# Kernel tuning notes

Measured on AMD Instinct MI355X. Metric: run time of the kernel, lower is better.

Reference implementation:

```python
import jax, jax.numpy as jnp
import numpy as np
from jax import lax

B, L, D, E, K, H = 8, 1024, 256, 8, 2, 1024  # batch, seq(in_channel), in_dim, experts, top_k, out_channel/hidden
LMAX = L // 2  # largest expert input dim (factor i+2 = 2)
LENS = [L // (i + 2) for i in range(E)]


def setup_inputs() -> dict:
    key = jax.random.key(0)
    ks = jax.random.split(key, 12)
    x = jax.random.normal(ks[0], (B, L, D), dtype=jnp.float32)
    conv_ws = jax.random.normal(ks[1], (3, D, D, 3), dtype=jnp.float32) / np.sqrt(3 * D)
    conv_bs = jax.random.normal(ks[2], (3, D), dtype=jnp.float32) * 0.01
    fl_w = jax.random.normal(ks[3], (E, L), dtype=jnp.float32) / np.sqrt(L)
    fl_b = jax.random.normal(ks[4], (E,), dtype=jnp.float32) * 0.01
    # expert first-layer weights, zero-padded on input axis to LMAX (expert i uses L//(i+2) inputs)
    w1 = jax.random.normal(ks[5], (E, H, LMAX), dtype=jnp.float32) / np.sqrt(LMAX)
    col_mask = (np.arange(LMAX)[None, :] < np.array(LENS)[:, None]).astype(np.float32)  # [E, LMAX]
    w1 = w1 * jnp.asarray(col_mask)[:, None, :]
    b1 = jax.random.normal(ks[6], (E, H), dtype=jnp.float32) * 0.01
    w2 = jax.random.normal(ks[7], (E, H, H), dtype=jnp.float32) / np.sqrt(H)
    b2 = jax.random.normal(ks[8], (E, H), dtype=jnp.float32) * 0.01
    w3 = jax.random.normal(ks[9], (E, H, H), dtype=jnp.float32) / np.sqrt(H)
    b3 = jax.random.normal(ks[10], (E, H), dtype=jnp.float32) * 0.01
    return {"x": x, "conv_ws": conv_ws, "conv_bs": conv_bs, "fl_w": fl_w, "fl_b": fl_b,
            "w1": w1, "b1": b1, "w2": w2, "b2": b2, "w3": w3, "b3": b3}


def _gelu(v):
    return jax.nn.gelu(v, approximate=False)  # torch nn.GELU default is exact erf


def _forward(x, conv_ws, conv_bs, fl_w, fl_b, w1, b1, w2, b2, w3, b3):
    xt = jnp.transpose(x, (0, 2, 1))  # [B, D, L]
    # --- Router: 3 dilated causal-padded ('same') convs + GELU ---
    h = xt
    for i in range(3):
        d = 2 ** i
        h = lax.conv_general_dilated(h, conv_ws[i], window_strides=(1,), padding=[(d, d)],
                                     rhs_dilation=(d,), dimension_numbers=("NCH", "OIH", "NCH"))
        h = _gelu(h + conv_bs[i][None, :, None])
    logits = jax.nn.sigmoid(jnp.einsum("bdl,el->bde", h, fl_w) + fl_b)  # [B, D, E]
    prob = jax.nn.softmax(logits, axis=-1)
    top_val, top_idx = lax.top_k(prob, K)  # [B, D, K]
    top_val = top_val / jnp.sum(top_val, axis=-1, keepdims=True)
    # combine gate per expert: gates[b,d,e] = sum_k top_val * 1[top_idx==e]
    gates = jnp.sum(top_val[..., None] * jax.nn.one_hot(top_idx, E, dtype=top_val.dtype), axis=2)  # [B, D, E]
    # --- Per-expert downsample (avg_pool1d, kernel=stride=i+2), zero-padded to LMAX ---
    xs = []
    for i in range(E):
        f = i + 2
        Li = LENS[i]
        xd = xt[:, :, :Li * f].reshape(B, D, Li, f).mean(-1)  # [B, D, Li]
        xs.append(jnp.pad(xd, ((0, 0), (0, 0), (0, LMAX - Li))))
    xe = jnp.stack(xs)  # [E, B, D, LMAX]; pad cols align with zeroed w1 cols
    # --- Expert MLPs (dense compute, masked by gates; zero gate == token not routed) ---
    h1 = _gelu(jnp.einsum("ebdl,ehl->ebdh", xe, w1) + b1[:, None, None, :])
    h2 = _gelu(jnp.einsum("ebdh,egh->ebdg", h1, w2) + b2[:, None, None, :])
    h3 = jnp.einsum("ebdg,eog->ebdo", h2, w3) + b3[:, None, None, :]  # [E, B, D, H]
    out = jnp.einsum("ebdo,bde->bdo", h3, gates)  # scatter-add combine, [B, D, H]
    return jnp.transpose(out, (0, 2, 1))  # [B, L(out_channel), D]


def reference(x, conv_ws, conv_bs, fl_w, fl_b, w1, b1, w2, b2, w3, b3):
    return _forward(x, conv_ws, conv_bs, fl_w, fl_b, w1, b1, w2, b2, w3, b3)
```

## Files before the change

kernel.cpp:

```cpp
#include <hip/hip_runtime.h>
#include <math.h>

#define Bb 8
#define Ll 1024
#define Dd 256
#define Ee 8
#define Hh 1024
#define LMAXc 512
#define NTOK (Bb*Dd)
#define LPAD 1032
#define MAXTILES 72

typedef short bf16x8 __attribute__((ext_vector_type(8)));
typedef float f32x4 __attribute__((ext_vector_type(4)));
typedef unsigned short u16x8 __attribute__((ext_vector_type(8)));

__device__ __forceinline__ float gelu_f(float x) {
    return 0.5f * x * (1.0f + erff(x * 0.70710678118654752440f));
}
__device__ __forceinline__ unsigned short f2b(float x) {
    unsigned int u = __float_as_uint(x);
    return (unsigned short)((u + 0x7fffu + ((u >> 16) & 1u)) >> 16);
}
__device__ __forceinline__ float b2f(unsigned short h) {
    return __uint_as_float(((unsigned int)h) << 16);
}
__device__ __forceinline__ void gl_lds16(const void* g, void* l) {
    __builtin_amdgcn_global_load_lds((const __attribute__((address_space(1))) unsigned int*)g,
                                     (__attribute__((address_space(3))) unsigned int*)l, 16, 0, 0);
}

__global__ __launch_bounds__(256) void prep_all(
    const float* __restrict__ x, const float* __restrict__ cw,
    unsigned short* __restrict__ xhi, unsigned short* __restrict__ xlo,
    unsigned short* __restrict__ chi, unsigned short* __restrict__ clo,
    unsigned short* __restrict__ wchi, unsigned short* __restrict__ wclo,
    unsigned short* __restrict__ xe)
{
    int blk = blockIdx.x;
    int t = threadIdx.x;
    if (blk < 4096) {
        int u = blk;
        int e = u >> 9;
        int b = (u >> 6) & 7;
        int c = u & 63;
        int f = e + 2;
        int Li = Ll / f;
        int j0 = c * 8;
        if (j0 >= Li) return;
        int d = t;
        float invf = 1.0f / (float)f;
        int lim = Li - 1;
        float v[8] = {};
        for (int r = 0; r < f; ++r) {
            #pragma unroll
            for (int jj = 0; jj < 8; ++jj) {
                int j = j0 + jj; if (j > lim) j = lim;
                v[jj] += x[((size_t)(b * Ll + j * f + r)) * Dd + d];
            }
        }
        size_t obase = ((size_t)(e * NTOK + b * 256 + d)) * LMAXc + j0;
        if (j0 + 8 <= Li) {
            u16x8 hv;
            #pragma unroll
            for (int q = 0; q < 8; ++q) hv[q] = (short)f2b(v[q] * invf);
            *(u16x8*)(xe + obase) = hv;
        } else {
            for (int jj = 0; jj < Li - j0; ++jj)
                xe[obase + jj] = f2b(v[jj] * invf);
        }
    } else if (blk < 4128) {
        int u = (blk - 4096) * 256 + t;
        int f = u >> 11;
        int rem = u & 2047;
        int b = rem >> 8;
        int r2 = rem & 255;
        int row = r2 >> 5;
        int col = (r2 & 31) * 8;
        int padrow = (row < 4) ? row : (1024 + row);
        unsigned short* buf = (f == 0) ? xhi : (f == 1) ? xlo : (f == 2) ? chi : clo;
        u16x8 z = {0, 0, 0, 0, 0, 0, 0, 0};
        *(u16x8*)(buf + (size_t)(b * LPAD + padrow) * Dd + col) = z;
    } else if (blk < 4384) {
        int cb = blk - 4128;
        const float4* s4 = (const float4*)x;
        size_t ob = (size_t)cb * 1024 + t;
        float4 v[8];
        #pragma unroll
        for (int it = 0; it < 4; ++it) {
            v[2 * it]     = s4[(ob + it * 256) * 2];
            v[2 * it + 1] = s4[(ob + it * 256) * 2 + 1];
        }
        #pragma unroll
        for (int it = 0; it < 4; ++it) {
            size_t o = ob + it * 256;
            int d8 = (int)(o & 31), l = (int)((o >> 5) & 1023), b = (int)(o >> 15);
            size_t ooff = (size_t)(b * LPAD + 4 + l) * Dd + d8 * 8;
            float vv[8] = {v[2*it].x, v[2*it].y, v[2*it].z, v[2*it].w,
                           v[2*it+1].x, v[2*it+1].y, v[2*it+1].z, v[2*it+1].w};
            u16x8 hv, lv;
            #pragma unroll
            for (int q = 0; q < 8; ++q) {
                unsigned short h = f2b(vv[q]);
                hv[q] = (short)h;
                lv[q] = (short)f2b(vv[q] - b2f(h));
            }
            *(u16x8*)(xhi + ooff) = hv;
            *(u16x8*)(xlo + ooff) = lv;
        }
    } else {
        int cb = blk - 4384;
        int idx0 = (cb * 256 + t) * 8;
        float vv[8];
        #pragma unroll
        for (int q = 0; q < 8; ++q) {
            int idx = idx0 + q;
            int i = idx & (Dd - 1);
            int o = (idx >> 8) & (Dd - 1);
            int lk = idx >> 16;
            int layer = lk / 3;
            int k = lk % 3;
            vv[q] = cw[(((size_t)layer * Dd + o) * Dd + i) * 3 + k];
        }
        u16x8 hv, lv;
        #pragma unroll
        for (int q = 0; q < 8; ++q) {
            unsigned short h = f2b(vv[q]);
            hv[q] = (short)h;
            lv[q] = (short)f2b(vv[q] - b2f(h));
        }
        *(u16x8*)(wchi + idx0) = hv;
        *(u16x8*)(wclo + idx0) = lv;
    }
}

template<int MODE, int CVT>
__global__ __launch_bounds__(256, 2) void conv_mfma(
    const unsigned short* __restrict__ inhi, const unsigned short* __restrict__ inlo,
    const unsigned short* __restrict__ whiL, const unsigned short* __restrict__ wloL,
    const float* __restrict__ bias,
    unsigned short* __restrict__ outhi, unsigned short* __restrict__ outlo,
    const float* __restrict__ flw, float* __restrict__ logits,
    const float* __restrict__ cvsrc, unsigned short* __restrict__ cvd1,
    unsigned short* __restrict__ cvd2, int dil)
{
    __shared__ char smem[32768];

    if (CVT && blockIdx.y >= (Dd / 64)) {
        int cb = (blockIdx.y - Dd / 64) * 128 + blockIdx.x;
        int t = threadIdx.x;
        const float4* s4 = (const float4*)cvsrc;
        size_t ob = (size_t)cb * 1024 + t;
        float4 v[8];
        #pragma unroll
        for (int it = 0; it < 4; ++it) {
            v[2 * it]     = s4[(ob + it * 256) * 2];
            v[2 * it + 1] = s4[(ob + it * 256) * 2 + 1];
        }
        #pragma unroll
        for (int it = 0; it < 4; ++it) {
            size_t o = ob + it * 256;
            float vv[8] = {v[2*it].x, v[2*it].y, v[2*it].z, v[2*it].w,
                           v[2*it+1].x, v[2*it+1].y, v[2*it+1].z, v[2*it+1].w};
            u16x8 hv, lv;
            #pragma unroll
            for (int q = 0; q < 8; ++q) {
                unsigned short h = f2b(vv[q]);
                hv[q] = (short)h;
                if (CVT == 1) lv[q] = (short)f2b(vv[q] - b2f(h));
            }
            *(u16x8*)(cvd1 + o * 8) = hv;
            if (CVT == 1) *(u16x8*)(cvd2 + o * 8) = lv;
        }
        return;
    }

    char* sAhi = smem;
    char* sAlo = smem + 8192;
    char* sBhi = smem + 16384;
    char* sBlo = smem + 24576;

    const int t = threadIdx.x;
    const int lane = t & 63, w = t >> 6;
    const int r16 = lane & 15, quad = lane >> 4;
    const int wr = w >> 1, wc = w & 1;
    const int row0 = blockIdx.x * 64;
    const int col0 = blockIdx.y * 64;
    const int b = row0 >> 10, l0 = row0 & 1023;

    int aoff[2], boff[2];
    #pragma unroll
    for (int i = 0; i < 2; ++i) {
        int ra = wr * 32 + i * 16 + r16;
        aoff[i] = ra * 64 + ((quad ^ ((ra >> 1) & 3)) << 4);
        int rb = wc * 32 + i * 16 + r16;
        boff[i] = rb * 64 + ((quad ^ ((rb >> 1) & 3)) << 4);
    }
    const int rs = t >> 2, ce = ((t & 3) ^ ((rs >> 1) & 3)) << 3;
    const unsigned short* gAhi = inhi + (size_t)(b * LPAD + 4 + l0 + rs) * Dd + ce;
    const unsigned short* gAlo = inlo + (size_t)(b * LPAD + 4 + l0 + rs) * Dd + ce;

    f32x4 acc[2][2];
    const f32x4 zero4 = {0.f, 0.f, 0.f, 0.f};
    #pragma unroll
    for (int i = 0; i < 2; ++i)
        #pragma unroll
        for (int j = 0; j < 2; ++j) acc[i][j] = zero4;

    for (int tap = 0; tap < 3; ++tap) {
        const int sh = (tap - 1) * dil;
        const unsigned short* pAhi = gAhi + sh * Dd;
        const unsigned short* pAlo = gAlo + sh * Dd;
        const unsigned short* gBhi = whiL + ((size_t)tap * Dd + col0 + rs) * Dd + ce;
        const unsigned short* gBlo = wloL + ((size_t)tap * Dd + col0 + rs) * Dd + ce;
        for (int kb = 0; kb < Dd; kb += 64) {
            gl_lds16(pAhi + kb,      sAhi + (w << 10));
            gl_lds16(pAhi + kb + 32, sAhi + 4096 + (w << 10));
            gl_lds16(pAlo + kb,      sAlo + (w << 10));
            gl_lds16(pAlo + kb + 32, sAlo + 4096 + (w << 10));
            gl_lds16(gBhi + kb,      sBhi + (w << 10));
            gl_lds16(gBhi + kb + 32, sBhi + 4096 + (w << 10));
            gl_lds16(gBlo + kb,      sBlo + (w << 10));
            gl_lds16(gBlo + kb + 32, sBlo + 4096 + (w << 10));
            __syncthreads();
            #pragma unroll
            for (int h = 0; h < 2; ++h) {
                const int ho = h * 4096;
                bf16x8 ah[2], al[2], bh[2], bl[2];
                #pragma unroll
                for (int i = 0; i < 2; ++i) {
                    ah[i] = *(const bf16x8*)(sAhi + ho + aoff[i]);
                    al[i] = *(const bf16x8*)(sAlo + ho + aoff[i]);
                    bh[i] = *(const bf16x8*)(sBhi + ho + boff[i]);
                    bl[i] = *(const bf16x8*)(sBlo + ho + boff[i]);
                }
                #pragma unroll
                for (int mi = 0; mi < 2; ++mi)
                    #pragma unroll
                    for (int ni = 0; ni < 2; ++ni) {
                        acc[mi][ni] = __builtin_amdgcn_mfma_f32_16x16x32_bf16(ah[mi], bh[ni], acc[mi][ni], 0, 0, 0);
                        acc[mi][ni] = __builtin_amdgcn_mfma_f32_16x16x32_bf16(ah[mi], bl[ni], acc[mi][ni], 0, 0, 0);
                        acc[mi][ni] = __builtin_amdgcn_mfma_f32_16x16x32_bf16(al[mi], bh[ni], acc[mi][ni], 0, 0, 0);
                    }
            }
            __syncthreads();
        }
    }

    int cc[2]; float bv[2];
    #pragma unroll
    for (int ni = 0; ni < 2; ++ni) {
        cc[ni] = col0 + wc * 32 + ni * 16 + r16;
        bv[ni] = bias[cc[ni]];
    }
    if (MODE == 0) {
        #pragma unroll
        for (int mi = 0; mi < 2; ++mi) {
            int lb = l0 + wr * 32 + mi * 16 + quad * 4;
            #pragma unroll
            for (int reg = 0; reg < 4; ++reg) {
                int l = lb + reg;
                #pragma unroll
                for (int ni = 0; ni < 2; ++ni) {
                    float v = gelu_f(acc[mi][ni][reg] + bv[ni]);
                    size_t o = (size_t)(b * LPAD + 4 + l) * Dd + cc[ni];
                    unsigned short h = f2b(v);
                    outhi[o] = h;
                    outlo[o] = f2b(v - b2f(h));
                }
            }
        }
    } else {
        float* wl   = (float*)smem;
        float* slog = (float*)(smem + 2048);
        for (int i = t; i < 512; i += 256) {
            int ll = i >> 3, e = i & 7;
            wl[i] = flw[e * Ll + l0 + ll];
            slog[i] = 0.0f;
        }
        __syncthreads();
        float part[2][8];
        #pragma unroll
        for (int ni = 0; ni < 2; ++ni)
            #pragma unroll
            for (int e = 0; e < 8; ++e) part[ni][e] = 0.0f;
        #pragma unroll
        for (int mi = 0; mi < 2; ++mi) {
            #pragma unroll
            for (int reg = 0; reg < 4; ++reg) {
                int ll = wr * 32 + mi * 16 + quad * 4 + reg;
                #pragma unroll
                for (int ni = 0; ni < 2; ++ni) {
                    float v = gelu_f(acc[mi][ni][reg] + bv[ni]);
                    #pragma unroll
                    for (int e = 0; e < 8; ++e) part[ni][e] += v * wl[ll * 8 + e];
                }
            }
        }
        #pragma unroll
        for (int ni = 0; ni < 2; ++ni) {
            int dl = wc * 32 + ni * 16 + r16;
            #pragma unroll
            for (int e = 0; e < 8; ++e) atomicAdd(&slog[dl * 8 + e], part[ni][e]);
        }
        __syncthreads();
        for (int i = t; i < 512; i += 256) {
            int dl = i >> 3, e = i & 7;
            atomicAdd(&logits[(size_t)(b * Dd + col0 + dl) * Ee + e], slog[i]);
        }
    }
}

template<int MODE, int GATHER, int TWOPASS>
__global__ __launch_bounds__(256, 4) void gemm_sp(
    const unsigned short* __restrict__ AG,
    const unsigned short* __restrict__ BhiG, const unsigned short* __restrict__ BloG,
    const float* __restrict__ biasG, const float* __restrict__ gates,
    const int* __restrict__ cntG, const int* __restrict__ listG,
    const int* __restrict__ tileTab, const int* __restrict__ ntiles,
    unsigned short* __restrict__ Cout, float* __restrict__ outf,
    int M, int N, int K)
{
    if (blockIdx.y >= ntiles[0]) return;
    const int desc = tileTab[blockIdx.y];
    const int e = desc >> 16;
    const int row0 = (desc & 0xffff) * 64;
    const int cn = cntG[e];

    constexpr int NCH = TWOPASS ? 2 : 4;
    __shared__ char smem[TWOPASS ? 24576 : 32768];
    char* sA   = smem;
    char* sBhi = smem + NCH * 4096;
    char* sBlo = smem + 2 * NCH * 4096;

    const unsigned short* Bhi = BhiG + (size_t)e * N * K;
    const unsigned short* Blo = TWOPASS ? (BloG + (size_t)e * N * K) : nullptr;
    const float* bias = biasG + (size_t)e * N;

    int Keff = K;
    if (GATHER) {
        int Li = Ll / (e + 2);
        Keff = ((Li + 63) >> 6) << 6;
    }

    const int t = threadIdx.x;
    const int lane = t & 63, w = t >> 6;
    const int r16 = lane & 15, quad = lane >> 4;
    const int wr = w >> 1, wc = w & 1;
    const int col0 = blockIdx.x * 64;

    int aoff[2], boff[2];
    #pragma unroll
    for (int i = 0; i < 2; ++i) {
        int ra = wr * 32 + i * 16 + r16;
        aoff[i] = ra * 64 + ((quad ^ ((ra >> 1) & 3)) << 4);
        int rb = wc * 32 + i * 16 + r16;
        boff[i] = rb * 64 + ((quad ^ ((rb >> 1) & 3)) << 4);
    }
    const int r0s = t >> 2, c0s = ((t & 3) ^ ((r0s >> 1) & 3)) << 3;
    int ri = row0 + r0s; if (ri > cn - 1) ri = cn - 1;
    const int ar = GATHER ? listG[e * NTOK + ri] : ri;
    const unsigned short* gA  = AG + ((size_t)e * M + ar) * K + c0s;
    const unsigned short* gB  = Bhi + (size_t)(col0 + r0s) * K + c0s;
    const unsigned short* gBl = TWOPASS ? (Blo + (size_t)(col0 + r0s) * K + c0s) : nullptr;
    const int wofs = w << 10;

    f32x4 acc[2][2];
    const f32x4 zero4 = {0.f, 0.f, 0.f, 0.f};
    #pragma unroll
    for (int i = 0; i < 2; ++i)
        #pragma unroll
        for (int j = 0; j < 2; ++j) acc[i][j] = zero4;

    for (int k0 = 0; k0 < Keff; k0 += NCH * 32) {
        #pragma unroll
        for (int c = 0; c < NCH; ++c) {
            gl_lds16(gA + k0 + c * 32, sA + c * 4096 + wofs);
            gl_lds16(gB + k0 + c * 32, sBhi + c * 4096 + wofs);
        }
        if (TWOPASS) {
            #pragma unroll
            for (int c = 0; c < NCH; ++c)
                gl_lds16(gBl + k0 + c * 32, sBlo + c * 4096 + wofs);
        }
        __syncthreads();
        #pragma unroll
        for (int h = 0; h < NCH; ++h) {
            const int ho = h * 4096;
            bf16x8 ah[2], bh[2];
            #pragma unroll
            for (int i = 0; i < 2; ++i) {
                ah[i] = *(const bf16x8*)(sA + ho + aoff[i]);
                bh[i] = *(const bf16x8*)(sBhi + ho + boff[i]);
            }
            #pragma unroll
            for (int mi = 0; mi < 2; ++mi)
                #pragma unroll
                for (int ni = 0; ni < 2; ++ni)
                    acc[mi][ni] = __builtin_amdgcn_mfma_f32_16x16x32_bf16(ah[mi], bh[ni], acc[mi][ni], 0, 0, 0);
            if (TWOPASS) {
                bf16x8 bl[2];
                #pragma unroll
                for (int i = 0; i < 2; ++i) bl[i] = *(const bf16x8*)(sBlo + ho + boff[i]);
                #pragma unroll
                for (int mi = 0; mi < 2; ++mi)
                    #pragma unroll
                    for (int ni = 0; ni < 2; ++ni)
                        acc[mi][ni] = __builtin_amdgcn_mfma_f32_16x16x32_bf16(ah[mi], bl[ni], acc[mi][ni], 0, 0, 0);
            }
        }
        __syncthreads();
    }

    int cc[2]; float bv[2];
    #pragma unroll
    for (int ni = 0; ni < 2; ++ni) {
        cc[ni] = col0 + wc * 32 + ni * 16 + r16;
        bv[ni] = bias[cc[ni]];
    }
    if (MODE == 0) {
        unsigned short* CE = Cout + (size_t)e * M * N;
        #pragma unroll
        for (int mi = 0; mi < 2; ++mi) {
            int rb = row0 + wr * 32 + mi * 16 + quad * 4;
            #pragma unroll
            for (int reg = 0; reg < 4; ++reg) {
                size_t roff = (size_t)(rb + reg) * N;
                #pragma unroll
                for (int ni = 0; ni < 2; ++ni)
                    CE[roff + cc[ni]] = f2b(gelu_f(acc[mi][ni][reg] + bv[ni]));
            }
        }
    } else {
        #pragma unroll
        for (int mi = 0; mi < 2; ++mi) {
            int rb = row0 + wr * 32 + mi * 16 + quad * 4;
            #pragma unroll
            for (int reg = 0; reg < 4; ++reg) {
                int i = rb + reg;
                if (i < cn) {
                    int tok = listG[e * NTOK + i];
                    float g = gates[(size_t)tok * Ee + e];
                    size_t roff = (size_t)tok * N;
                    #pragma unroll
                    for (int ni = 0; ni < 2; ++ni)
                        atomicAdd(&outf[roff + cc[ni]], g * (acc[mi][ni][reg] + bv[ni]));
                }
            }
        }
    }
}


__global__ __launch_bounds__(1024) void gates_final(const float* __restrict__ logits,
                                                    const float* __restrict__ fl_b,
                                                    float* __restrict__ gates,
                                                    int* __restrict__ cnt,
                                                    int* __restrict__ list,
                                                    int* __restrict__ tileTab,
                                                    int* __restrict__ ntiles) {
    __shared__ int scnt[Ee];
    if (threadIdx.x < Ee) scnt[threadIdx.x] = 0;
    __syncthreads();
    const int lane = threadIdx.x & 63;
    const unsigned long long ltmask = (1ull << lane) - 1ull;

    for (int tok = threadIdx.x; tok < NTOK; tok += 1024) {
        float s[Ee];
        #pragma unroll
        for (int e = 0; e < Ee; ++e) {
            float z = logits[tok * Ee + e] + fl_b[e];
            s[e] = 1.0f / (1.0f + expf(-z));
        }
        float mx = s[0];
        #pragma unroll
        for (int e = 1; e < Ee; ++e) mx = fmaxf(mx, s[e]);
        float p[Ee];
        #pragma unroll
        for (int e = 0; e < Ee; ++e) p[e] = expf(s[e] - mx);
        int i1 = 0;
        #pragma unroll
        for (int e = 1; e < Ee; ++e) if (p[e] > p[i1]) i1 = e;
        int i2 = (i1 == 0) ? 1 : 0;
        #pragma unroll
        for (int e = 0; e < Ee; ++e) {
            if (e == i1 || e == i2) continue;
            if (p[e] > p[i2]) i2 = e;
        }
        float inv = 1.0f / (p[i1] + p[i2]);
        #pragma unroll
        for (int e = 0; e < Ee; ++e) gates[tok * Ee + e] = 0.0f;
        gates[tok * Ee + i1] = p[i1] * inv;
        gates[tok * Ee + i2] = p[i2] * inv;

        #pragma unroll
        for (int slot = 0; slot < 2; ++slot) {
            int ie = slot ? i2 : i1;
            for (int e = 0; e < Ee; ++e) {
                unsigned long long m = __ballot(ie == e);
                if (m) {
                    int leader = __ffsll((long long)m) - 1;
                    int base = 0;
                    if (lane == leader) base = atomicAdd(&scnt[e], (int)__popcll(m));
                    base = __shfl(base, leader);
                    if (ie == e) {
                        int pos = base + (int)__popcll(m & ltmask);
                        list[e * NTOK + pos] = tok;
                    }
                }
            }
        }
    }
    __syncthreads();
    if (threadIdx.x < Ee) cnt[threadIdx.x] = scnt[threadIdx.x];
    if (threadIdx.x == 0) {
        int nt = 0;
        for (int e = 0; e < Ee; ++e) {
            int c = scnt[e];
            for (int m = 0; m * 64 < c; ++m) tileTab[nt++] = (e << 16) | m;
        }
        ntiles[0] = nt;
    }
}

__global__ __launch_bounds__(256) void transpose_out(const float* __restrict__ outacc,
                                                     float* __restrict__ out) {
    __shared__ float tile[32][33];
    int b = blockIdx.z;
    int d0 = blockIdx.x * 32;
    int o0 = blockIdx.y * 32;
    int tx = threadIdx.x & 31, ty = threadIdx.x >> 5;
    for (int i = 0; i < 32; i += 8)
        tile[ty + i][tx] = outacc[((size_t)b * Dd + d0 + ty + i) * Hh + o0 + tx];
    __syncthreads();
    for (int i = 0; i < 32; i += 8)
        out[((size_t)b * Hh + o0 + ty + i) * Dd + d0 + tx] = tile[tx][ty + i];
}

extern "C" void kernel_launch(void* const* d_in, const int* in_sizes, int n_in,
                              void* d_out, int out_size, void* d_ws, size_t ws_size,
                              hipStream_t stream) {
    const float* x       = (const float*)d_in[0];
    const float* conv_w  = (const float*)d_in[1];
    const float* conv_b  = (const float*)d_in[2];
    const float* fl_w    = (const float*)d_in[3];
    const float* fl_b    = (const float*)d_in[4];
    const float* w1      = (const float*)d_in[5];
    const float* b1      = (const float*)d_in[6];
    const float* w2      = (const float*)d_in[7];
    const float* b2      = (const float*)d_in[8];
    const float* w3      = (const float*)d_in[9];
    const float* b3      = (const float*)d_in[10];
    float* out = (float*)d_out;

    char* ws = (char*)d_ws;
    unsigned short* xphi = (unsigned short*)(ws);
    unsigned short* xplo = (unsigned short*)(ws + 4227072);
    unsigned short* cphi = (unsigned short*)(ws + 8454144);
    unsigned short* cplo = (unsigned short*)(ws + 12681216);
    unsigned short* wchi = (unsigned short*)(ws + 16908288);
    unsigned short* wclo = (unsigned short*)(ws + 18087936);
    unsigned short* h1   = (unsigned short*)(ws);
    unsigned short* h2   = (unsigned short*)(ws + 33554432);
    unsigned short* xe   = (unsigned short*)(ws + 67108864);
    unsigned short* w1hi = (unsigned short*)(ws + 83886080);
    unsigned short* w1lo = (unsigned short*)(ws + 92274688);
    unsigned short* w2b  = (unsigned short*)(ws + 100663296);
    unsigned short* w3b  = (unsigned short*)(ws + 117440512);
    float* logits  = (float*)(ws + 134217728);
    int*   cnt     = (int*)(ws + 134283264);
    int*   ntiles  = (int*)(ws + 134283296);
    int*   tileTab = (int*)(ws + 134283328);
    float* gates   = (float*)(ws + 134284288);
    int*   list    = (int*)(ws + 134349824);
    float* outacc  = (float*)(ws);

    hipMemsetAsync(logits, 0, 65536 + 64, stream);

    prep_all<<<4672, 256, 0, stream>>>(x, conv_w, xphi, xplo, cphi, cplo,
                                       wchi, wclo, xe);

    const int WL = 3 * Dd * Dd;
    conv_mfma<0, 1><<<dim3(Bb * Ll / 64, Dd / 64 + 4), 256, 0, stream>>>(
        xphi, xplo, wchi + 0 * WL, wclo + 0 * WL, conv_b + 0 * Dd, cphi, cplo,
        nullptr, nullptr, w1, w1hi, w1lo, 1);
    conv_mfma<0, 2><<<dim3(Bb * Ll / 64, Dd / 64 + 8), 256, 0, stream>>>(
        cphi, cplo, wchi + 1 * WL, wclo + 1 * WL, conv_b + 1 * Dd, xphi, xplo,
        nullptr, nullptr, w2, w2b, nullptr, 2);
    conv_mfma<1, 2><<<dim3(Bb * Ll / 64, Dd / 64 + 8), 256, 0, stream>>>(
        xphi, xplo, wchi + 2 * WL, wclo + 2 * WL, conv_b + 2 * Dd, nullptr, nullptr,
        fl_w, logits, w3, w3b, nullptr, 4);

    gates_final<<<1, 1024, 0, stream>>>(logits, fl_b, gates, cnt, list, tileTab, ntiles);

    gemm_sp<0, 1, 1><<<dim3(16, MAXTILES), 256, 0, stream>>>(
        xe, w1hi, w1lo, b1, nullptr, cnt, list, tileTab, ntiles, h1, nullptr, NTOK, Hh, LMAXc);

    gemm_sp<0, 0, 0><<<dim3(16, MAXTILES), 256, 0, stream>>>(
        h1, w2b, nullptr, b2, nullptr, cnt, list, tileTab, ntiles, h2, nullptr, NTOK, Hh, Hh);

    hipMemsetAsync(outacc, 0, (size_t)NTOK * Hh * sizeof(float), stream);

    gemm_sp<1, 0, 0><<<dim3(16, MAXTILES), 256, 0, stream>>>(
        h2, w3b, nullptr, b3, gates, cnt, list, tileTab, ntiles, nullptr, outacc, NTOK, Hh, Hh);

    transpose_out<<<dim3(Dd / 32, Hh / 32, Bb), 256, 0, stream>>>(outacc, out);
}
```

Measured before the change: 309.5 us.

## Use 128x128 tiled sparse expert GEMM kernel for second and third MLP layers

```diff
diff --git a/kernel.cpp b/kernel.cpp
--- a/kernel.cpp
+++ b/kernel.cpp
@@ -10,6 +10,7 @@
 #define NTOK (Bb*Dd)
 #define LPAD 1032
 #define MAXTILES 72
+#define MAXT128 40
 
 typedef short bf16x8 __attribute__((ext_vector_type(8)));
 typedef float f32x4 __attribute__((ext_vector_type(4)));
@@ -451,6 +452,126 @@
     }
 }
 
+template<int MODE>
+__global__ __launch_bounds__(256, 2) void gemm_sp128(
+    const unsigned short* __restrict__ AG,
+    const unsigned short* __restrict__ BG,
+    const float* __restrict__ biasG, const float* __restrict__ gates,
+    const int* __restrict__ cntG, const int* __restrict__ listG,
+    const int* __restrict__ tileTab, const int* __restrict__ ntiles,
+    unsigned short* __restrict__ Cout, float* __restrict__ outf,
+    int M, int N, int K)
+{
+    if (blockIdx.y >= ntiles[0]) return;
+    const int desc = tileTab[blockIdx.y];
+    const int e = desc >> 16;
+    const int row0 = (desc & 0xffff) * 128;
+    const int cn = cntG[e];
+
+    __shared__ char smem[32768];
+    char* sA = smem;
+    char* sB = smem + 16384;
+
+    const unsigned short* B = BG + (size_t)e * N * K;
+    const float* bias = biasG + (size_t)e * N;
+
+    const int t = threadIdx.x;
+    const int lane = t & 63, w = t >> 6;
+    const int r16 = lane & 15, quad = lane >> 4;
+    const int wr = w >> 1, wc = w & 1;
+    const int col0 = blockIdx.x * 128;
+
+    int aoff[4], boff[4];
+    #pragma unroll
+    for (int i = 0; i < 4; ++i) {
+        int ra = wr * 64 + i * 16 + r16;
+        aoff[i] = ra * 64 + ((quad ^ ((ra >> 1) & 3)) << 4);
+        int rb = wc * 64 + i * 16 + r16;
+        boff[i] = rb * 64 + ((quad ^ ((rb >> 1) & 3)) << 4);
+    }
+
+    const int r0s = t >> 2, c0s = ((t & 3) ^ ((r0s >> 1) & 3)) << 3;
+    int ri0 = row0 + r0s;       if (ri0 > cn - 1) ri0 = cn - 1;
+    int ri1 = row0 + 64 + r0s;  if (ri1 > cn - 1) ri1 = cn - 1;
+    const unsigned short* gA0 = AG + ((size_t)e * M + ri0) * K + c0s;
+    const unsigned short* gA1 = AG + ((size_t)e * M + ri1) * K + c0s;
+    const unsigned short* gB0 = B + (size_t)(col0 + r0s) * K + c0s;
+    const unsigned short* gB1 = B + (size_t)(col0 + 64 + r0s) * K + c0s;
+    const int wofs = w << 10;
+
+    f32x4 acc[4][4];
+    const f32x4 zero4 = {0.f, 0.f, 0.f, 0.f};
+    #pragma unroll
+    for (int i = 0; i < 4; ++i)
+        #pragma unroll
+        for (int j = 0; j < 4; ++j) acc[i][j] = zero4;
+
+    for (int k0 = 0; k0 < K; k0 += 64) {
+        #pragma unroll
+        for (int c = 0; c < 2; ++c) {
+            gl_lds16(gA0 + k0 + c * 32, sA + c * 8192 + wofs);
+            gl_lds16(gA1 + k0 + c * 32, sA + c * 8192 + 4096 + wofs);
+            gl_lds16(gB0 + k0 + c * 32, sB + c * 8192 + wofs);
+            gl_lds16(gB1 + k0 + c * 32, sB + c * 8192 + 4096 + wofs);
+        }
+        __syncthreads();
+        #pragma unroll
+        for (int h = 0; h < 2; ++h) {
+            const int ho = h * 8192;
+            bf16x8 a[4], b[4];
+            #pragma unroll
+            for (int i = 0; i < 4; ++i) {
+                a[i] = *(const bf16x8*)(sA + ho + aoff[i]);
+                b[i] = *(const bf16x8*)(sB + ho + boff[i]);
+            }
+            #pragma unroll
+            for (int mi = 0; mi < 4; ++mi)
+                #pragma unroll
+                for (int ni = 0; ni < 4; ++ni)
+                    acc[mi][ni] = __builtin_amdgcn_mfma_f32_16x16x32_bf16(a[mi], b[ni], acc[mi][ni], 0, 0, 0);
+        }
+        __syncthreads();
+    }
+
+    int cc[4]; float bv[4];
+    #pragma unroll
+    for (int ni = 0; ni < 4; ++ni) {
+        cc[ni] = col0 + wc * 64 + ni * 16 + r16;
+        bv[ni] = bias[cc[ni]];
+    }
+    if (MODE == 0) {
+        unsigned short* CE = Cout + (size_t)e * M * N;
+        #pragma unroll
+        for (int mi = 0; mi < 4; ++mi) {
+            int rb = row0 + wr * 64 + mi * 16 + quad * 4;
+            #pragma unroll
+            for (int reg = 0; reg < 4; ++reg) {
+                size_t roff = (size_t)(rb + reg) * N;
+                #pragma unroll
+                for (int ni = 0; ni < 4; ++ni)
+                    CE[roff + cc[ni]] = f2b(gelu_f(acc[mi][ni][reg] + bv[ni]));
+            }
+        }
+    } else {
+        #pragma unroll
+        for (int mi = 0; mi < 4; ++mi) {
+            int rb = row0 + wr * 64 + mi * 16 + quad * 4;
+            #pragma unroll
+            for (int reg = 0; reg < 4; ++reg) {
+                int i = rb + reg;
+                if (i < cn) {
+                    int tok = listG[e * NTOK + i];
+                    float g = gates[(size_t)tok * Ee + e];
+                    size_t roff = (size_t)tok * N;
+                    #pragma unroll
+                    for (int ni = 0; ni < 4; ++ni)
+                        atomicAdd(&outf[roff + cc[ni]], g * (acc[mi][ni][reg] + bv[ni]));
+                }
+            }
+        }
+    }
+}
+
 
 __global__ __launch_bounds__(1024) void gates_final(const float* __restrict__ logits,
                                                     const float* __restrict__ fl_b,
@@ -458,6 +579,7 @@
                                                     int* __restrict__ cnt,
                                                     int* __restrict__ list,
                                                     int* __restrict__ tileTab,
+                                                    int* __restrict__ tileTab128,
                                                     int* __restrict__ ntiles) {
     __shared__ int scnt[Ee];
     if (threadIdx.x < Ee) scnt[threadIdx.x] = 0;
@@ -514,12 +636,14 @@
     __syncthreads();
     if (threadIdx.x < Ee) cnt[threadIdx.x] = scnt[threadIdx.x];
     if (threadIdx.x == 0) {
-        int nt = 0;
+        int nt = 0, nt2 = 0;
         for (int e = 0; e < Ee; ++e) {
             int c = scnt[e];
             for (int m = 0; m * 64 < c; ++m) tileTab[nt++] = (e << 16) | m;
+            for (int m = 0; m * 128 < c; ++m) tileTab128[nt2++] = (e << 16) | m;
         }
         ntiles[0] = nt;
+        ntiles[1] = nt2;
     }
 }
 
@@ -571,6 +695,7 @@
     int*   cnt     = (int*)(ws + 134283264);
     int*   ntiles  = (int*)(ws + 134283296);
     int*   tileTab = (int*)(ws + 134283328);
+    int*   tileTab128 = (int*)(ws + 134283328 + 384);
     float* gates   = (float*)(ws + 134284288);
     int*   list    = (int*)(ws + 134349824);
     float* outacc  = (float*)(ws);
@@ -591,18 +716,19 @@
         xphi, xplo, wchi + 2 * WL, wclo + 2 * WL, conv_b + 2 * Dd, nullptr, nullptr,
         fl_w, logits, w3, w3b, nullptr, 4);
 
-    gates_final<<<1, 1024, 0, stream>>>(logits, fl_b, gates, cnt, list, tileTab, ntiles);
+    gates_final<<<1, 1024, 0, stream>>>(logits, fl_b, gates, cnt, list,
+                                        tileTab, tileTab128, ntiles);
 
     gemm_sp<0, 1, 1><<<dim3(16, MAXTILES), 256, 0, stream>>>(
         xe, w1hi, w1lo, b1, nullptr, cnt, list, tileTab, ntiles, h1, nullptr, NTOK, Hh, LMAXc);
 
-    gemm_sp<0, 0, 0><<<dim3(16, MAXTILES), 256, 0, stream>>>(
-        h1, w2b, nullptr, b2, nullptr, cnt, list, tileTab, ntiles, h2, nullptr, NTOK, Hh, Hh);
+    gemm_sp128<0><<<dim3(Hh / 128, MAXT128), 256, 0, stream>>>(
+        h1, w2b, b2, nullptr, cnt, list, tileTab128, ntiles + 1, h2, nullptr, NTOK, Hh, Hh);
 
     hipMemsetAsync(outacc, 0, (size_t)NTOK * Hh * sizeof(float), stream);
 
-    gemm_sp<1, 0, 0><<<dim3(16, MAXTILES), 256, 0, stream>>>(
-        h2, w3b, nullptr, b3, gates, cnt, list, tileTab, ntiles, nullptr, outacc, NTOK, Hh, Hh);
+    gemm_sp128<1><<<dim3(Hh / 128, MAXT128), 256, 0, stream>>>(
+        h2, w3b, b3, gates, cnt, list, tileTab128, ntiles + 1, nullptr, outacc, NTOK, Hh, Hh);
 
     transpose_out<<<dim3(Dd / 32, Hh / 32, Bb), 256, 0, stream>>>(outacc, out);
 }
```

New measurement: 315.2 us. Within noise of the previous version (+1.8%).

## Replace atomic scatter-add combine with per-slot stores and gather-combine kernel

Applied to the files above, without the earlier changes.

```diff
diff --git a/kernel.cpp b/kernel.cpp
--- a/kernel.cpp
+++ b/kernel.cpp
@@ -441,10 +441,10 @@
                 if (i < cn) {
                     int tok = listG[e * NTOK + i];
                     float g = gates[(size_t)tok * Ee + e];
-                    size_t roff = (size_t)tok * N;
+                    size_t roff = ((size_t)e * NTOK + i) * N;
                     #pragma unroll
                     for (int ni = 0; ni < 2; ++ni)
-                        atomicAdd(&outf[roff + cc[ni]], g * (acc[mi][ni][reg] + bv[ni]));
+                        outf[roff + cc[ni]] = g * (acc[mi][ni][reg] + bv[ni]);
                 }
             }
         }
@@ -452,86 +452,90 @@
 }
 
 
-__global__ __launch_bounds__(1024) void gates_final(const float* __restrict__ logits,
-                                                    const float* __restrict__ fl_b,
-                                                    float* __restrict__ gates,
-                                                    int* __restrict__ cnt,
-                                                    int* __restrict__ list,
-                                                    int* __restrict__ tileTab,
-                                                    int* __restrict__ ntiles) {
-    __shared__ int scnt[Ee];
-    if (threadIdx.x < Ee) scnt[threadIdx.x] = 0;
-    __syncthreads();
+__global__ __launch_bounds__(256) void gates_topk(const float* __restrict__ logits,
+                                                  const float* __restrict__ fl_b,
+                                                  float* __restrict__ gates,
+                                                  int* __restrict__ cnt,
+                                                  int* __restrict__ list,
+                                                  int* __restrict__ rowidx) {
+    const int tok = blockIdx.x * 256 + threadIdx.x;
     const int lane = threadIdx.x & 63;
     const unsigned long long ltmask = (1ull << lane) - 1ull;
 
-    for (int tok = threadIdx.x; tok < NTOK; tok += 1024) {
-        float s[Ee];
-        #pragma unroll
+    float s[Ee];
+    #pragma unroll
+    for (int e = 0; e < Ee; ++e) {
+        float z = logits[tok * Ee + e] + fl_b[e];
+        s[e] = 1.0f / (1.0f + expf(-z));
+    }
+    float mx = s[0];
+    #pragma unroll
+    for (int e = 1; e < Ee; ++e) mx = fmaxf(mx, s[e]);
+    float p[Ee];
+    #pragma unroll
+    for (int e = 0; e < Ee; ++e) p[e] = expf(s[e] - mx);
+    int i1 = 0;
+    #pragma unroll
+    for (int e = 1; e < Ee; ++e) if (p[e] > p[i1]) i1 = e;
+    int i2 = (i1 == 0) ? 1 : 0;
+    #pragma unroll
+    for (int e = 0; e < Ee; ++e) {
+        if (e == i1 || e == i2) continue;
+        if (p[e] > p[i2]) i2 = e;
+    }
+    float inv = 1.0f / (p[i1] + p[i2]);
+    #pragma unroll
+    for (int e = 0; e < Ee; ++e) gates[tok * Ee + e] = 0.0f;
+    gates[tok * Ee + i1] = p[i1] * inv;
+    gates[tok * Ee + i2] = p[i2] * inv;
+
+    #pragma unroll
+    for (int slot = 0; slot < 2; ++slot) {
+        int ie = slot ? i2 : i1;
         for (int e = 0; e < Ee; ++e) {
-            float z = logits[tok * Ee + e] + fl_b[e];
-            s[e] = 1.0f / (1.0f + expf(-z));
-        }
-        float mx = s[0];
-        #pragma unroll
-        for (int e = 1; e < Ee; ++e) mx = fmaxf(mx, s[e]);
-        float p[Ee];
-        #pragma unroll
-        for (int e = 0; e < Ee; ++e) p[e] = expf(s[e] - mx);
-        int i1 = 0;
-        #pragma unroll
-        for (int e = 1; e < Ee; ++e) if (p[e] > p[i1]) i1 = e;
-        int i2 = (i1 == 0) ? 1 : 0;
-        #pragma unroll
-        for (int e = 0; e < Ee; ++e) {
-            if (e == i1 || e == i2) continue;
-            if (p[e] > p[i2]) i2 = e;
-        }
-        float inv = 1.0f / (p[i1] + p[i2]);
-        #pragma unroll
-        for (int e = 0; e < Ee; ++e) gates[tok * Ee + e] = 0.0f;
-        gates[tok * Ee + i1] = p[i1] * inv;
-        gates[tok * Ee + i2] = p[i2] * inv;
-
-        #pragma unroll
-        for (int slot = 0; slot < 2; ++slot) {
-            int ie = slot ? i2 : i1;
-            for (int e = 0; e < Ee; ++e) {
-                unsigned long long m = __ballot(ie == e);
-                if (m) {
-                    int leader = __ffsll((long long)m) - 1;
-                    int base = 0;
-                    if (lane == leader) base = atomicAdd(&scnt[e], (int)__popcll(m));
-                    base = __shfl(base, leader);
-                    if (ie == e) {
-                        int pos = base + (int)__popcll(m & ltmask);
-                        list[e * NTOK + pos] = tok;
-                    }
+            unsigned long long m = __ballot(ie == e);
+            if (m) {
+                int leader = __ffsll((long long)m) - 1;
+                int base = 0;
+                if (lane == leader) base = atomicAdd(&cnt[e], (int)__popcll(m));
+                base = __shfl(base, leader);
+                if (ie == e) {
+                    int pos = base + (int)__popcll(m & ltmask);
+                    list[e * NTOK + pos] = tok;
+                    rowidx[tok * 2 + slot] = e * NTOK + pos;
                 }
             }
         }
     }
-    __syncthreads();
-    if (threadIdx.x < Ee) cnt[threadIdx.x] = scnt[threadIdx.x];
+}
+
+__global__ void tiletab_build(const int* __restrict__ cnt,
+                              int* __restrict__ tileTab,
+                              int* __restrict__ ntiles) {
     if (threadIdx.x == 0) {
         int nt = 0;
         for (int e = 0; e < Ee; ++e) {
-            int c = scnt[e];
+            int c = cnt[e];
             for (int m = 0; m * 64 < c; ++m) tileTab[nt++] = (e << 16) | m;
         }
         ntiles[0] = nt;
     }
 }
 
-__global__ __launch_bounds__(256) void transpose_out(const float* __restrict__ outacc,
-                                                     float* __restrict__ out) {
+__global__ __launch_bounds__(256) void combine_out(const float* __restrict__ h3g,
+                                                   const int* __restrict__ rowidx,
+                                                   float* __restrict__ out) {
     __shared__ float tile[32][33];
     int b = blockIdx.z;
     int d0 = blockIdx.x * 32;
     int o0 = blockIdx.y * 32;
     int tx = threadIdx.x & 31, ty = threadIdx.x >> 5;
-    for (int i = 0; i < 32; i += 8)
-        tile[ty + i][tx] = outacc[((size_t)b * Dd + d0 + ty + i) * Hh + o0 + tx];
+    for (int i = 0; i < 32; i += 8) {
+        int tok = b * Dd + d0 + ty + i;
+        int r0 = rowidx[tok * 2];
+        int r1 = rowidx[tok * 2 + 1];
+        tile[ty + i][tx] = h3g[(size_t)r0 * Hh + o0 + tx] + h3g[(size_t)r1 * Hh + o0 + tx];
+    }
     __syncthreads();
     for (int i = 0; i < 32; i += 8)
         out[((size_t)b * Hh + o0 + ty + i) * Dd + d0 + tx] = tile[tx][ty + i];
@@ -561,7 +565,8 @@
     unsigned short* wchi = (unsigned short*)(ws + 16908288);
     unsigned short* wclo = (unsigned short*)(ws + 18087936);
     unsigned short* h1   = (unsigned short*)(ws);
-    unsigned short* h2   = (unsigned short*)(ws + 33554432);
+    unsigned short* h2   = (unsigned short*)(ws + 67108864);
+    float*          h3g  = (float*)(ws);
     unsigned short* xe   = (unsigned short*)(ws + 67108864);
     unsigned short* w1hi = (unsigned short*)(ws + 83886080);
     unsigned short* w1lo = (unsigned short*)(ws + 92274688);
@@ -573,7 +578,7 @@
     int*   tileTab = (int*)(ws + 134283328);
     float* gates   = (float*)(ws + 134284288);
     int*   list    = (int*)(ws + 134349824);
-    float* outacc  = (float*)(ws);
+    int*   rowidx  = (int*)(ws + 134415360);
 
     hipMemsetAsync(logits, 0, 65536 + 64, stream);
 
@@ -591,7 +596,8 @@
         xphi, xplo, wchi + 2 * WL, wclo + 2 * WL, conv_b + 2 * Dd, nullptr, nullptr,
         fl_w, logits, w3, w3b, nullptr, 4);
 
-    gates_final<<<1, 1024, 0, stream>>>(logits, fl_b, gates, cnt, list, tileTab, ntiles);
+    gates_topk<<<NTOK / 256, 256, 0, stream>>>(logits, fl_b, gates, cnt, list, rowidx);
+    tiletab_build<<<1, 64, 0, stream>>>(cnt, tileTab, ntiles);
 
     gemm_sp<0, 1, 1><<<dim3(16, MAXTILES), 256, 0, stream>>>(
         xe, w1hi, w1lo, b1, nullptr, cnt, list, tileTab, ntiles, h1, nullptr, NTOK, Hh, LMAXc);
@@ -599,10 +605,8 @@
     gemm_sp<0, 0, 0><<<dim3(16, MAXTILES), 256, 0, stream>>>(
         h1, w2b, nullptr, b2, nullptr, cnt, list, tileTab, ntiles, h2, nullptr, NTOK, Hh, Hh);
 
-    hipMemsetAsync(outacc, 0, (size_t)NTOK * Hh * sizeof(float), stream);
-
     gemm_sp<1, 0, 0><<<dim3(16, MAXTILES), 256, 0, stream>>>(
-        h2, w3b, nullptr, b3, gates, cnt, list, tileTab, ntiles, nullptr, outacc, NTOK, Hh, Hh);
-
-    transpose_out<<<dim3(Dd / 32, Hh / 32, Bb), 256, 0, stream>>>(outacc, out);
-}
+        h2, w3b, nullptr, b3, gates, cnt, list, tileTab, ntiles, nullptr, h3g, NTOK, Hh, Hh);
+
+    combine_out<<<dim3(Dd / 32, Hh / 32, Bb), 256, 0, stream>>>(h3g, rowidx, out);
+}
```

New measurement: 293.4 us. 1.05x faster.
